# Performance work log

Measured on AMD Instinct MI355X. Metric: run time of the kernel, lower is better.

The kernel has to match this reference:

```python
import jax, jax.numpy as jnp
import numpy as np

D_MODEL = 512
NUM_HEADS = 8
HEAD_DIM = D_MODEL // NUM_HEADS
WINDOW = 64


def setup_inputs() -> dict:
    key = jax.random.key(0)
    ks = jax.random.split(key, 9)
    B, L = 4, 2048
    s = 1.0 / np.sqrt(D_MODEL)
    return {
        "x": jax.random.normal(ks[0], (B, L, D_MODEL), dtype=jnp.float32),
        "Wq": jax.random.normal(ks[1], (D_MODEL, D_MODEL), dtype=jnp.float32) * s,
        "bq": jnp.zeros((D_MODEL,), jnp.float32),
        "Wk": jax.random.normal(ks[2], (D_MODEL, D_MODEL), dtype=jnp.float32) * s,
        "bk": jnp.zeros((D_MODEL,), jnp.float32),
        "Wv": jax.random.normal(ks[3], (D_MODEL, D_MODEL), dtype=jnp.float32) * s,
        "bv": jnp.zeros((D_MODEL,), jnp.float32),
        "Wo": jax.random.normal(ks[4], (D_MODEL, D_MODEL), dtype=jnp.float32) * s,
        "bo": jnp.zeros((D_MODEL,), jnp.float32),
    }


def reference(x, Wq, bq, Wk, bk, Wv, bv, Wo, bo):
    B, L, _ = x.shape
    # projections -> [B, H, L, Dh]
    def proj(W, b):
        return (x @ W + b).reshape(B, L, NUM_HEADS, HEAD_DIM).transpose(0, 2, 1, 3)
    q, k, v = proj(Wq, bq), proj(Wk, bk), proj(Wv, bv)
    scores = jnp.einsum("bhqd,bhkd->bhqk", q, k) / np.sqrt(HEAD_DIM)
    idx = jnp.arange(L)
    dist = jnp.abs(idx[None, :] - idx[:, None])  # [L, L]
    mask = dist > WINDOW
    scores = jnp.where(mask[None, None], -jnp.inf, scores)
    attn = jax.nn.softmax(scores, axis=-1)  # dropout p inert in eval
    out = jnp.einsum("bhqk,bhkd->bhqd", attn, v)
    out = out.transpose(0, 2, 1, 3).reshape(B, L, D_MODEL)
    return out @ Wo + bo
```

## Files before the change

kernel.cpp:

```cpp
#include <hip/hip_runtime.h>
#include <cstdint>
#include <cstddef>

typedef _Float16 f16;
typedef f16 f16x8 __attribute__((ext_vector_type(8)));
typedef f16 f16x4 __attribute__((ext_vector_type(4)));
typedef float floatx4 __attribute__((ext_vector_type(4)));

#define GAS __attribute__((address_space(1)))
#define LAS __attribute__((address_space(3)))

static constexpr int LSEQ = 2048;
static constexpr int NH   = 8;
static constexpr int DH   = 64;
static constexpr int DM   = 512;
static constexpr int WIN  = 64;
static constexpr int MR   = 4 * LSEQ;

__global__ __launch_bounds__(256) void prep_kernel(
    const float* __restrict__ x, f16* __restrict__ xb,
    const float* __restrict__ Wq, const float* __restrict__ Wk,
    const float* __restrict__ Wv, const float* __restrict__ Wo,
    f16* __restrict__ wt) {
    __shared__ float tile[32][33];
    int bid = blockIdx.x;
    if (bid < 4096) {
        int i = bid * 256 + threadIdx.x;
        float4 v = ((const float4*)x)[i];
        f16x4 o = { (f16)v.x, (f16)v.y, (f16)v.z, (f16)v.w };
        ((f16x4*)xb)[i] = o;
    } else {
        int id = bid - 4096;
        int z  = id >> 8, t = id & 255;
        const float* W = z == 0 ? Wq : z == 1 ? Wk : z == 2 ? Wv : Wo;
        f16* out = wt + (size_t)z * DM * DM;
        int c0 = (t & 15) * 32, r0 = (t >> 4) * 32;
        int tx = threadIdx.x & 31, ty = threadIdx.x >> 5;
        #pragma unroll
        for (int i = 0; i < 32; i += 8)
            tile[ty + i][tx] = W[(size_t)(r0 + ty + i) * DM + c0 + tx];
        __syncthreads();
        #pragma unroll
        for (int i = 0; i < 32; i += 8)
            out[(size_t)(c0 + ty + i) * DM + r0 + tx] = (f16)tile[tx][ty + i];
    }
}

template <bool QKV>
__global__ __launch_bounds__(256) void gemm_kernel(
    const f16* __restrict__ A, const f16* __restrict__ Bt_base,
    const float* __restrict__ b0, const float* __restrict__ b1,
    const float* __restrict__ b2,
    f16* __restrict__ out_q, f16* __restrict__ out_k, f16* __restrict__ out_vt,
    float* __restrict__ out_f) {
    const int chunk = gridDim.x >> 3;
    const int hw  = blockIdx.x;
    const int lin = (hw & 7) * chunk + (hw >> 3);
    const int n0  = (lin & 7) * 64;
    const int m0  = ((lin >> 3) & 31) * 256;
    const int z   = QKV ? (lin >> 8) : 0;

    const f16* __restrict__ Bt = Bt_base + (size_t)z * (DM * DM);
    const float* __restrict__ bias = QKV ? (z == 0 ? b0 : z == 1 ? b1 : b2) : b0;

    __shared__ f16 Bs[64 * 512];

    const int tid  = threadIdx.x;
    const int wid  = tid >> 6;
    const int lane = tid & 63;
    const int l15  = lane & 15;
    const int l4   = lane >> 4;
    const int rbase = m0 + wid * 64;

    #pragma unroll
    for (int i = 0; i < 16; ++i) {
        int gg  = i * 256 + tid;
        int col = gg >> 6, gp = gg & 63;
        int sg  = gp ^ (col & 7);
        const f16* g = Bt + (size_t)(n0 + col) * DM + sg * 8;
        f16* l = &Bs[(i * 256 + wid * 64) * 8];
        __builtin_amdgcn_global_load_lds((const GAS void*)g, (LAS void*)l, 16, 0, 0);
    }
    __syncthreads();

    floatx4 acc[4][4] = {};

    #pragma unroll 4
    for (int ks = 0; ks < 16; ++ks) {
        f16x8 af[4], bfr[4];
        #pragma unroll
        for (int m = 0; m < 4; ++m)
            af[m] = *(const f16x8*)(A + (size_t)(rbase + m * 16 + l15) * DM + ks * 32 + l4 * 8);
        #pragma unroll
        for (int n = 0; n < 4; ++n) {
            int col = n * 16 + l15;
            int gp  = (ks * 4 + l4) ^ (col & 7);
            bfr[n] = *(const f16x8*)(&Bs[col * 512 + gp * 8]);
        }
        #pragma unroll
        for (int m = 0; m < 4; ++m)
            #pragma unroll
            for (int n = 0; n < 4; ++n)
                acc[m][n] = __builtin_amdgcn_mfma_f32_16x16x32_f16(af[m], bfr[n], acc[m][n], 0, 0, 0);
    }

    #pragma unroll
    for (int n = 0; n < 4; ++n) {
        int gcol = n0 + n * 16 + l15;
        float bias_v = bias[gcol];
        #pragma unroll
        for (int m = 0; m < 4; ++m) {
            int grow0 = rbase + m * 16 + l4 * 4;
            #pragma unroll
            for (int r = 0; r < 4; ++r) {
                int grow = grow0 + r;
                float v = acc[m][n][r] + bias_v;
                if constexpr (QKV) {
                    int b = grow >> 11, lp = grow & (LSEQ - 1);
                    int h = gcol >> 6,  d  = gcol & (DH - 1);
                    int bh = b * NH + h;
                    if (z == 0)
                        out_q[((size_t)bh * LSEQ + lp) * DH + d] = (f16)(v * 0.125f);
                    else if (z == 1)
                        out_k[((size_t)bh * LSEQ + lp) * DH + d] = (f16)v;
                    else
                        out_vt[((size_t)bh * DH + d) * LSEQ + lp] = (f16)v;
                } else {
                    out_f[(size_t)grow * DM + gcol] = v;
                }
            }
        }
    }
}

__global__ __launch_bounds__(256) void attn_kernel(const f16* __restrict__ Qb,
                                                   const f16* __restrict__ Kb,
                                                   const f16* __restrict__ Vt,
                                                   f16* __restrict__ Ob) {
    const int hw  = blockIdx.x;
    const int lin = (hw & 7) * 128 + (hw >> 3);
    const int bh    = lin >> 5;
    const int q0blk = (lin & 31) * 64;
    const int wid    = threadIdx.x >> 6;
    const int lane   = threadIdx.x & 63;
    const int l15    = lane & 15, l4 = lane >> 4;
    const int qbase  = q0blk + wid * 16;
    const int kstart = q0blk - WIN;

    const f16* __restrict__ Q = Qb + (size_t)bh * LSEQ * DH;
    const f16* __restrict__ K = Kb + (size_t)bh * LSEQ * DH;
    const f16* __restrict__ V = Vt + (size_t)bh * DH * LSEQ;

    __shared__ f16 Pl[4][16][232];

    f16x8 qf[2];
    #pragma unroll
    for (int ks = 0; ks < 2; ++ks)
        qf[ks] = *(const f16x8*)(Q + (size_t)(qbase + l15) * DH + ks * 32 + l4 * 8);

    floatx4 sc[12] = {};
    #pragma unroll
    for (int nt = 0; nt < 12; ++nt) {
        int key = kstart + nt * 16 + l15;
        int kcl = key < 0 ? 0 : (key > LSEQ - 1 ? LSEQ - 1 : key);
        #pragma unroll
        for (int ks = 0; ks < 2; ++ks) {
            f16x8 kf = *(const f16x8*)(K + (size_t)kcl * DH + ks * 32 + l4 * 8);
            sc[nt] = __builtin_amdgcn_mfma_f32_16x16x32_f16(qf[ks], kf, sc[nt], 0, 0, 0);
        }
    }

    float mx[4] = {-1e30f, -1e30f, -1e30f, -1e30f};
    #pragma unroll
    for (int nt = 0; nt < 12; ++nt) {
        int key = kstart + nt * 16 + l15;
        #pragma unroll
        for (int r = 0; r < 4; ++r) {
            int q = qbase + l4 * 4 + r;
            int dist = key - q; dist = dist < 0 ? -dist : dist;
            bool valid = (key >= 0) && (key < LSEQ) && (dist <= WIN);
            float s = valid ? sc[nt][r] : -1e30f;
            sc[nt][r] = s;
            mx[r] = fmaxf(mx[r], s);
        }
    }
    #pragma unroll
    for (int r = 0; r < 4; ++r)
        #pragma unroll
        for (int m = 1; m < 16; m <<= 1)
            mx[r] = fmaxf(mx[r], __shfl_xor(mx[r], m, 64));
    float sm[4] = {0.f, 0.f, 0.f, 0.f};
    #pragma unroll
    for (int nt = 0; nt < 12; ++nt)
        #pragma unroll
        for (int r = 0; r < 4; ++r) {
            float p = __expf(sc[nt][r] - mx[r]);
            sc[nt][r] = p;
            sm[r] += p;
        }
    #pragma unroll
    for (int r = 0; r < 4; ++r) {
        #pragma unroll
        for (int m = 1; m < 16; m <<= 1)
            sm[r] += __shfl_xor(sm[r], m, 64);
        sm[r] = 1.f / sm[r];
    }

    #pragma unroll
    for (int nt = 0; nt < 12; ++nt)
        #pragma unroll
        for (int r = 0; r < 4; ++r)
            Pl[wid][l4 * 4 + r][nt * 16 + l15] = (f16)(sc[nt][r] * sm[r]);
    __syncthreads();

    floatx4 oc[4] = {};
    #pragma unroll
    for (int ks = 0; ks < 6; ++ks) {
        f16x8 pf = *(const f16x8*)(&Pl[wid][l15][ks * 32 + l4 * 8]);
        int kb0 = kstart + ks * 32 + l4 * 8;
        int kbc = (kb0 < 0 || kb0 > LSEQ - 8) ? 0 : kb0;
        #pragma unroll
        for (int dt = 0; dt < 4; ++dt) {
            f16x8 vf = *(const f16x8*)(V + (size_t)(dt * 16 + l15) * LSEQ + kbc);
            oc[dt] = __builtin_amdgcn_mfma_f32_16x16x32_f16(pf, vf, oc[dt], 0, 0, 0);
        }
    }

    int b = bh >> 3, h = bh & 7;
    #pragma unroll
    for (int dt = 0; dt < 4; ++dt) {
        int d = dt * 16 + l15;
        #pragma unroll
        for (int r = 0; r < 4; ++r) {
            int q = qbase + l4 * 4 + r;
            Ob[((size_t)b * LSEQ + q) * DM + h * DH + d] = (f16)oc[dt][r];
        }
    }
}

extern "C" void kernel_launch(void* const* d_in, const int* in_sizes, int n_in,
                              void* d_out, int out_size, void* d_ws, size_t ws_size,
                              hipStream_t stream) {
    const float* x  = (const float*)d_in[0];
    const float* Wq = (const float*)d_in[1];
    const float* bq = (const float*)d_in[2];
    const float* Wk = (const float*)d_in[3];
    const float* bk = (const float*)d_in[4];
    const float* Wv = (const float*)d_in[5];
    const float* bv = (const float*)d_in[6];
    const float* Wo = (const float*)d_in[7];
    const float* bo = (const float*)d_in[8];
    float* out = (float*)d_out;

    char* ws = (char*)d_ws;
    f16* xb = (f16*)(ws);
    f16* wt = (f16*)(ws + (8ull << 20));
    f16* qb = (f16*)(ws + (10ull << 20));
    f16* kb = (f16*)(ws + (18ull << 20));
    f16* vt = (f16*)(ws + (26ull << 20));
    f16* ob = (f16*)(ws + (34ull << 20));

    prep_kernel<<<dim3(5120), 256, 0, stream>>>(x, xb, Wq, Wk, Wv, Wo, wt);
    gemm_kernel<true><<<dim3(768), 256, 0, stream>>>(
        xb, wt, bq, bk, bv, qb, kb, vt, nullptr);
    attn_kernel<<<dim3(1024), 256, 0, stream>>>(qb, kb, vt, ob);
    gemm_kernel<false><<<dim3(256), 256, 0, stream>>>(
        ob, wt + 3ull * DM * DM, bo, bo, bo, nullptr, nullptr, nullptr, out);
}
```

Baseline: 101.6 us.

## Restructure projection GEMMs to stage A rows in LDS and stream weights from global

The GEMM tiling is swapped. Each block now covers all 512 output columns for a small slab of rows (64 for QKV, 32 for the output projection), using 512 threads. The A slab is staged in swizzled LDS, and the B (weight) fragments are read straight from global/L2. Before, a 64-column weight tile sat in LDS and the A rows were read directly from global. The aim is to read each activation row once per block instead of eight times across the column tiles, and to rely on the small, L2-resident weights for the B operand. In exchange, B-operand loads now go through global memory inside the MFMA loop, and the grid changes to 384 and 256 blocks of 512 threads.

```diff
diff --git a/kernel.cpp b/kernel.cpp
--- a/kernel.cpp
+++ b/kernel.cpp
@@ -47,58 +47,61 @@
 }
 
 template <bool QKV>
-__global__ __launch_bounds__(256) void gemm_kernel(
+__global__ __launch_bounds__(512, 4) void gemm_kernel(
     const f16* __restrict__ A, const f16* __restrict__ Bt_base,
     const float* __restrict__ b0, const float* __restrict__ b1,
     const float* __restrict__ b2,
     f16* __restrict__ out_q, f16* __restrict__ out_k, f16* __restrict__ out_vt,
     float* __restrict__ out_f) {
+    constexpr int BM = QKV ? 64 : 32;
+    constexpr int MF = BM / 16;
+    constexpr int GR = BM * 64;
     const int chunk = gridDim.x >> 3;
     const int hw  = blockIdx.x;
     const int lin = (hw & 7) * chunk + (hw >> 3);
-    const int n0  = (lin & 7) * 64;
-    const int m0  = ((lin >> 3) & 31) * 256;
-    const int z   = QKV ? (lin >> 8) : 0;
+    const int m0  = (QKV ? (lin & 127) : lin) * BM;
+    const int z   = QKV ? (lin >> 7) : 0;
 
     const f16* __restrict__ Bt = Bt_base + (size_t)z * (DM * DM);
     const float* __restrict__ bias = QKV ? (z == 0 ? b0 : z == 1 ? b1 : b2) : b0;
 
-    __shared__ f16 Bs[64 * 512];
+    __shared__ f16 As[BM * DM];
 
     const int tid  = threadIdx.x;
     const int wid  = tid >> 6;
     const int lane = tid & 63;
     const int l15  = lane & 15;
     const int l4   = lane >> 4;
-    const int rbase = m0 + wid * 64;
-
-    #pragma unroll
-    for (int i = 0; i < 16; ++i) {
-        int gg  = i * 256 + tid;
-        int col = gg >> 6, gp = gg & 63;
-        int sg  = gp ^ (col & 7);
-        const f16* g = Bt + (size_t)(n0 + col) * DM + sg * 8;
-        f16* l = &Bs[(i * 256 + wid * 64) * 8];
+
+    #pragma unroll
+    for (int i = 0; i < GR / 512; ++i) {
+        int gg  = i * 512 + tid;
+        int row = gg >> 6, gp = gg & 63;
+        int sg  = gp ^ (row & 7);
+        const f16* g = A + (size_t)(m0 + row) * DM + sg * 8;
+        f16* l = &As[(i * 512 + wid * 64) * 8];
         __builtin_amdgcn_global_load_lds((const GAS void*)g, (LAS void*)l, 16, 0, 0);
     }
     __syncthreads();
 
-    floatx4 acc[4][4] = {};
+    floatx4 acc[MF][4] = {};
 
     #pragma unroll 4
     for (int ks = 0; ks < 16; ++ks) {
-        f16x8 af[4], bfr[4];
-        #pragma unroll
-        for (int m = 0; m < 4; ++m)
-            af[m] = *(const f16x8*)(A + (size_t)(rbase + m * 16 + l15) * DM + ks * 32 + l4 * 8);
+        f16x8 af[MF], bfr[4];
+        #pragma unroll
+        for (int m = 0; m < MF; ++m) {
+            int row = m * 16 + l15;
+            int gp  = (ks * 4 + l4) ^ (row & 7);
+            af[m] = *(const f16x8*)(&As[row * DM + gp * 8]);
+        }
         #pragma unroll
         for (int n = 0; n < 4; ++n) {
-            int col = n * 16 + l15;
-            int gp  = (ks * 4 + l4) ^ (col & 7);
-            bfr[n] = *(const f16x8*)(&Bs[col * 512 + gp * 8]);
-        }
-        #pragma unroll
-        for (int m = 0; m < 4; ++m)
+            int col = wid * 64 + n * 16 + l15;
+            bfr[n] = *(const f16x8*)(Bt + (size_t)col * DM + (ks * 4 + l4) * 8);
+        }
+        #pragma unroll
+        for (int m = 0; m < MF; ++m)
             #pragma unroll
             for (int n = 0; n < 4; ++n)
                 acc[m][n] = __builtin_amdgcn_mfma_f32_16x16x32_f16(af[m], bfr[n], acc[m][n], 0, 0, 0);
@@ -106,11 +109,11 @@
 
     #pragma unroll
     for (int n = 0; n < 4; ++n) {
-        int gcol = n0 + n * 16 + l15;
+        int gcol = wid * 64 + n * 16 + l15;
         float bias_v = bias[gcol];
         #pragma unroll
-        for (int m = 0; m < 4; ++m) {
-            int grow0 = rbase + m * 16 + l4 * 4;
+        for (int m = 0; m < MF; ++m) {
+            int grow0 = m0 + m * 16 + l4 * 4;
             #pragma unroll
             for (int r = 0; r < 4; ++r) {
                 int grow = grow0 + r;
@@ -261,9 +264,9 @@
     f16* ob = (f16*)(ws + (34ull << 20));
 
     prep_kernel<<<dim3(5120), 256, 0, stream>>>(x, xb, Wq, Wk, Wv, Wo, wt);
-    gemm_kernel<true><<<dim3(768), 256, 0, stream>>>(
+    gemm_kernel<true><<<dim3(384), 512, 0, stream>>>(
         xb, wt, bq, bk, bv, qb, kb, vt, nullptr);
     attn_kernel<<<dim3(1024), 256, 0, stream>>>(qb, kb, vt, ob);
-    gemm_kernel<false><<<dim3(256), 256, 0, stream>>>(
+    gemm_kernel<false><<<dim3(256), 512, 0, stream>>>(
         ob, wt + 3ull * DM * DM, bo, bo, bo, nullptr, nullptr, nullptr, out);
 }
```

New measurement: 115.5 us. 13.6% more time.

## Prepack weights in MFMA fragment order and load B directly from global

Applied to the files above, without the earlier changes.

The weight prep now writes each weight matrix in an MFMA-fragment-packed layout, so each lane's 16-byte B fragment is contiguous. The GEMM drops the LDS staging of the full 64x512 B tile and the barrier, and each wave reads B fragments straight from global/L2. Waves become independent tiles, with occupancy hinted via launch bounds. The output projection uses 32-row wave tiles and twice as many blocks for more parallelism. This trades LDS reuse for more global/L2 traffic on B fragments, and the prep transpose now writes with poor coalescing.

```diff
diff --git a/kernel.cpp b/kernel.cpp
--- a/kernel.cpp
+++ b/kernel.cpp
@@ -6,9 +6,6 @@
 typedef f16 f16x8 __attribute__((ext_vector_type(8)));
 typedef f16 f16x4 __attribute__((ext_vector_type(4)));
 typedef float floatx4 __attribute__((ext_vector_type(4)));
-
-#define GAS __attribute__((address_space(1)))
-#define LAS __attribute__((address_space(3)))
 
 static constexpr int LSEQ = 2048;
 static constexpr int NH   = 8;
@@ -22,7 +19,6 @@
     const float* __restrict__ Wq, const float* __restrict__ Wk,
     const float* __restrict__ Wv, const float* __restrict__ Wo,
     f16* __restrict__ wt) {
-    __shared__ float tile[32][33];
     int bid = blockIdx.x;
     if (bid < 4096) {
         int i = bid * 256 + threadIdx.x;
@@ -31,85 +27,72 @@
         ((f16x4*)xb)[i] = o;
     } else {
         int id = bid - 4096;
-        int z  = id >> 8, t = id & 255;
+        int z  = id >> 5, ct16 = id & 31;
         const float* W = z == 0 ? Wq : z == 1 ? Wk : z == 2 ? Wv : Wo;
-        f16* out = wt + (size_t)z * DM * DM;
-        int c0 = (t & 15) * 32, r0 = (t >> 4) * 32;
-        int tx = threadIdx.x & 31, ty = threadIdx.x >> 5;
-        #pragma unroll
-        for (int i = 0; i < 32; i += 8)
-            tile[ty + i][tx] = W[(size_t)(r0 + ty + i) * DM + c0 + tx];
-        __syncthreads();
-        #pragma unroll
-        for (int i = 0; i < 32; i += 8)
-            out[(size_t)(c0 + ty + i) * DM + r0 + tx] = (f16)tile[tx][ty + i];
+        f16* dst = wt + (size_t)z * DM * DM;
+        #pragma unroll
+        for (int i = 0; i < 32; ++i) {
+            int idx = i * 256 + threadIdx.x;
+            int c15 = idx & 15, k = idx >> 4;
+            int ks = k >> 5, l4k = (k >> 3) & 3, w = k & 7;
+            float v = W[(size_t)k * DM + ct16 * 16 + c15];
+            dst[(size_t)(ct16 * 16 + ks) * 512 + (l4k * 16 + c15) * 8 + w] = (f16)v;
+        }
     }
 }
 
 template <bool QKV>
-__global__ __launch_bounds__(256) void gemm_kernel(
-    const f16* __restrict__ A, const f16* __restrict__ Bt_base,
+__global__ __launch_bounds__(256, 4) void gemm_kernel(
+    const f16* __restrict__ A, const f16* __restrict__ Bp_base,
     const float* __restrict__ b0, const float* __restrict__ b1,
     const float* __restrict__ b2,
     f16* __restrict__ out_q, f16* __restrict__ out_k, f16* __restrict__ out_vt,
     float* __restrict__ out_f) {
+    constexpr int MF = QKV ? 4 : 2;
     const int chunk = gridDim.x >> 3;
     const int hw  = blockIdx.x;
     const int lin = (hw & 7) * chunk + (hw >> 3);
-    const int n0  = (lin & 7) * 64;
-    const int m0  = ((lin >> 3) & 31) * 256;
-    const int z   = QKV ? (lin >> 8) : 0;
-
-    const f16* __restrict__ Bt = Bt_base + (size_t)z * (DM * DM);
+    const int wid  = threadIdx.x >> 6;
+    const int lane = threadIdx.x & 63;
+    const int wave = lin * 4 + wid;
+    int z, rt, ct;
+    if constexpr (QKV) { z = wave >> 10; int rem = wave & 1023; rt = rem >> 3; ct = rem & 7; }
+    else               { z = 0; rt = wave >> 3; ct = wave & 7; }
+    const int rbase = rt * (MF * 16);
+    const int l15 = lane & 15, l4 = lane >> 4;
+
+    const f16* __restrict__ pk = Bp_base + (size_t)z * DM * DM + (size_t)(ct * 4) * 16 * 512;
     const float* __restrict__ bias = QKV ? (z == 0 ? b0 : z == 1 ? b1 : b2) : b0;
 
-    __shared__ f16 Bs[64 * 512];
-
-    const int tid  = threadIdx.x;
-    const int wid  = tid >> 6;
-    const int lane = tid & 63;
-    const int l15  = lane & 15;
-    const int l4   = lane >> 4;
-    const int rbase = m0 + wid * 64;
-
-    #pragma unroll
-    for (int i = 0; i < 16; ++i) {
-        int gg  = i * 256 + tid;
-        int col = gg >> 6, gp = gg & 63;
-        int sg  = gp ^ (col & 7);
-        const f16* g = Bt + (size_t)(n0 + col) * DM + sg * 8;
-        f16* l = &Bs[(i * 256 + wid * 64) * 8];
-        __builtin_amdgcn_global_load_lds((const GAS void*)g, (LAS void*)l, 16, 0, 0);
-    }
-    __syncthreads();
-
-    floatx4 acc[4][4] = {};
-
-    #pragma unroll 4
+    const f16* arow[MF];
+    #pragma unroll
+    for (int m = 0; m < MF; ++m)
+        arow[m] = A + (size_t)(rbase + m * 16 + l15) * DM + l4 * 8;
+
+    floatx4 acc[MF][4] = {};
+
+    #pragma unroll 2
     for (int ks = 0; ks < 16; ++ks) {
-        f16x8 af[4], bfr[4];
-        #pragma unroll
-        for (int m = 0; m < 4; ++m)
-            af[m] = *(const f16x8*)(A + (size_t)(rbase + m * 16 + l15) * DM + ks * 32 + l4 * 8);
-        #pragma unroll
-        for (int n = 0; n < 4; ++n) {
-            int col = n * 16 + l15;
-            int gp  = (ks * 4 + l4) ^ (col & 7);
-            bfr[n] = *(const f16x8*)(&Bs[col * 512 + gp * 8]);
-        }
-        #pragma unroll
-        for (int m = 0; m < 4; ++m)
+        f16x8 af[MF], bf[4];
+        #pragma unroll
+        for (int m = 0; m < MF; ++m)
+            af[m] = *(const f16x8*)(arow[m] + ks * 32);
+        #pragma unroll
+        for (int n = 0; n < 4; ++n)
+            bf[n] = *(const f16x8*)(pk + (size_t)(n * 16 + ks) * 512 + lane * 8);
+        #pragma unroll
+        for (int m = 0; m < MF; ++m)
             #pragma unroll
             for (int n = 0; n < 4; ++n)
-                acc[m][n] = __builtin_amdgcn_mfma_f32_16x16x32_f16(af[m], bfr[n], acc[m][n], 0, 0, 0);
+                acc[m][n] = __builtin_amdgcn_mfma_f32_16x16x32_f16(af[m], bf[n], acc[m][n], 0, 0, 0);
     }
 
     #pragma unroll
     for (int n = 0; n < 4; ++n) {
-        int gcol = n0 + n * 16 + l15;
+        int gcol = ct * 64 + n * 16 + l15;
         float bias_v = bias[gcol];
         #pragma unroll
-        for (int m = 0; m < 4; ++m) {
+        for (int m = 0; m < MF; ++m) {
             int grow0 = rbase + m * 16 + l4 * 4;
             #pragma unroll
             for (int r = 0; r < 4; ++r) {
@@ -260,10 +243,10 @@
     f16* vt = (f16*)(ws + (26ull << 20));
     f16* ob = (f16*)(ws + (34ull << 20));
 
-    prep_kernel<<<dim3(5120), 256, 0, stream>>>(x, xb, Wq, Wk, Wv, Wo, wt);
+    prep_kernel<<<dim3(4224), 256, 0, stream>>>(x, xb, Wq, Wk, Wv, Wo, wt);
     gemm_kernel<true><<<dim3(768), 256, 0, stream>>>(
         xb, wt, bq, bk, bv, qb, kb, vt, nullptr);
     attn_kernel<<<dim3(1024), 256, 0, stream>>>(qb, kb, vt, ob);
-    gemm_kernel<false><<<dim3(256), 256, 0, stream>>>(
+    gemm_kernel<false><<<dim3(512), 256, 0, stream>>>(
         ob, wt + 3ull * DM * DM, bo, bo, bo, nullptr, nullptr, nullptr, out);
 }
```

After: 110.6 us. +8.9%, slower.
